# Optimization experiments

Hardware: AMD Instinct MI355X
Metric: run time of the kernel (lower is better)

The kernel has to match this reference:

```python
import jax, jax.numpy as jnp
import numpy as np

B, N, C, K = 1024, 100, 256, 3  # batch, num_proposals, hidden_dim, conv kernel size
LN_EPS = 1e-5


def setup_inputs() -> dict:
    key = jax.random.key(0)
    k1, k2, k3 = jax.random.split(key, 3)
    query = jax.random.normal(k1, (B, N, C), dtype=jnp.float32)
    value = jax.random.normal(k2, (B, N, C), dtype=jnp.float32)
    # weight_linear: Linear(hidden_dim -> kernel_size)
    W_w = jax.random.normal(k3, (K, C), dtype=jnp.float32) * (1.0 / np.sqrt(C))
    b_w = jnp.zeros((K,), dtype=jnp.float32)
    # LayerNorm(hidden_dim)
    gamma = jnp.ones((C,), dtype=jnp.float32)
    beta = jnp.zeros((C,), dtype=jnp.float32)
    return {"query": query, "value": value, "W_w": W_w, "b_w": b_w,
            "gamma": gamma, "beta": beta}


def reference(query, value, W_w, b_w, gamma, beta):
    Bq, Nq, Cq = query.shape
    Kk = W_w.shape[0]
    # dynamic depthwise kernels: [B, N, K]
    w = jnp.einsum('bnc,kc->bnk', query, W_w) + b_w
    # torch conv1d with padding='same' (cross-correlation along C, groups=N)
    pad_l = (Kk - 1) // 2
    pad_r = Kk // 2
    vpad = jnp.pad(value, ((0, 0), (0, 0), (pad_l, pad_r)))
    # sliding windows along channel axis: [B, N, C, K]
    win = jnp.stack([vpad[:, :, k:k + Cq] for k in range(Kk)], axis=-1)
    out = jnp.einsum('bnck,bnk->bnc', win, w)
    # LayerNorm over last dim
    mu = jnp.mean(out, axis=-1, keepdims=True)
    var = jnp.mean(jnp.square(out - mu), axis=-1, keepdims=True)
    out = (out - mu) * jax.lax.rsqrt(var + LN_EPS) * gamma + beta
    return out
```

## Files before the change

### kernel.cpp

```cpp
#include <hip/hip_runtime.h>

constexpr int B = 1024, N = 100, C = 256, K = 3;
constexpr int ROWS = B * N;
constexpr int THREADS = 256;
constexpr int WAVES_PER_BLOCK = THREADS / 64;
constexpr int BLOCKS = 2048;
constexpr int TOTAL_WAVES = BLOCKS * WAVES_PER_BLOCK;
constexpr float LN_EPS = 1e-5f;

typedef float f32x4 __attribute__((ext_vector_type(4)));

template <int N_>
__device__ __forceinline__ float fror(float x) {
    return __int_as_float(__builtin_amdgcn_update_dpp(
        0, __float_as_int(x), 0x120 | N_, 0xF, 0xF, false));
}

__device__ __forceinline__ float wavesum(float x) {
    x += fror<1>(x);
    x += fror<2>(x);
    x += fror<4>(x);
    x += fror<8>(x);
    x += __shfl_xor(x, 16);
    x += __shfl_xor(x, 32);
    return x;
}

__global__ __launch_bounds__(256) void dydwconv_ln_kernel(
    const float* __restrict__ query,
    const float* __restrict__ value,
    const float* __restrict__ Ww,
    const float* __restrict__ bw,
    const float* __restrict__ gamma,
    const float* __restrict__ beta,
    float* __restrict__ out)
{
    const int t    = threadIdx.x;
    const int lane = t & 63;
    const int c0   = lane * 4;
    const int row0 = blockIdx.x * WAVES_PER_BLOCK + (t >> 6);

    const int nIter = (ROWS - row0 + TOTAL_WAVES - 1) / TOTAL_WAVES;

    const float4 Wa = *(const float4*)(Ww + c0);
    const float4 Wb = *(const float4*)(Ww + C + c0);
    const float4 Wc = *(const float4*)(Ww + 2 * C + c0);
    const float4 g4 = *(const float4*)(gamma + c0);
    const float4 b4 = *(const float4*)(beta + c0);
    const float  b0 = bw[0], b1 = bw[1], b2 = bw[2];

    constexpr size_t STEP = (size_t)TOTAL_WAVES * C;
    size_t off = (size_t)row0 * C + c0;

    float4 qc = *(const float4*)(query + off);
    float4 vc = *(const float4*)(value + off);

    for (int it = 0; it < nIter; ++it) {
        const bool hn = (it + 1) < nIter;
        const size_t noff = off + STEP;
        float4 qn = qc, vn = vc;
        if (hn) {
            qn = *(const float4*)(query + noff);
            vn = *(const float4*)(value + noff);
        }

        float p0 = qc.x * Wa.x + qc.y * Wa.y + qc.z * Wa.z + qc.w * Wa.w;
        float p1 = qc.x * Wb.x + qc.y * Wb.y + qc.z * Wb.z + qc.w * Wb.w;
        float p2 = qc.x * Wc.x + qc.y * Wc.y + qc.z * Wc.z + qc.w * Wc.w;
        const float w0 = wavesum(p0) + b0;
        const float w1 = wavesum(p1) + b1;
        const float w2 = wavesum(p2) + b2;

        float vl = __shfl_up(vc.w, 1);
        float vr = __shfl_down(vc.x, 1);
        if (lane == 0)  vl = 0.0f;
        if (lane == 63) vr = 0.0f;

        const float o0 = vl   * w0 + vc.x * w1 + vc.y * w2;
        const float o1 = vc.x * w0 + vc.y * w1 + vc.z * w2;
        const float o2 = vc.y * w0 + vc.z * w1 + vc.w * w2;
        const float o3 = vc.z * w0 + vc.w * w1 + vr   * w2;

        float s  = (o0 + o1) + (o2 + o3);
        float ss = o0 * o0 + o1 * o1 + o2 * o2 + o3 * o3;
        s  = wavesum(s);
        ss = wavesum(ss);
        const float mu  = s * (1.0f / C);
        const float var = ss * (1.0f / C) - mu * mu;
        const float inv = rsqrtf(var + LN_EPS);

        f32x4 r;
        r.x = (o0 - mu) * inv * g4.x + b4.x;
        r.y = (o1 - mu) * inv * g4.y + b4.y;
        r.z = (o2 - mu) * inv * g4.z + b4.z;
        r.w = (o3 - mu) * inv * g4.w + b4.w;
        __builtin_nontemporal_store(r, (f32x4*)(out + off));

        off = noff;
        qc = qn;
        vc = vn;
    }
}

extern "C" void kernel_launch(void* const* d_in, const int* in_sizes, int n_in,
                              void* d_out, int out_size, void* d_ws, size_t ws_size,
                              hipStream_t stream) {
    const float* query = (const float*)d_in[0];
    const float* value = (const float*)d_in[1];
    const float* Ww    = (const float*)d_in[2];
    const float* bw    = (const float*)d_in[3];
    const float* gamma = (const float*)d_in[4];
    const float* beta  = (const float*)d_in[5];
    float* outp = (float*)d_out;

    dydwconv_ln_kernel<<<BLOCKS, THREADS, 0, stream>>>(
        query, value, Ww, bw, gamma, beta, outp);
}
```

Baseline: 262.6 us.

## Process four rows per wave with batched loads instead of grid-stride loop

Replaces the persistent grid-stride loop over rows with a non-persistent grid in which each wave handles four consecutive rows. All loads for those rows are issued up front, and their reductions are batched so that independent shuffles can interleave. The DPP-based wave reduction is replaced with plain shfl_xor, and nontemporal stores become regular stores. This gives more memory-level parallelism per wave, at the cost of a much larger grid, more registers, and slower shuffle-based reductions.

After: 256.5 us. 1.02x faster.

```diff
diff --git a/kernel.cpp b/kernel.cpp
--- a/kernel.cpp
+++ b/kernel.cpp
@@ -3,26 +3,15 @@
 constexpr int B = 1024, N = 100, C = 256, K = 3;
 constexpr int ROWS = B * N;
 constexpr int THREADS = 256;
-constexpr int WAVES_PER_BLOCK = THREADS / 64;
-constexpr int BLOCKS = 2048;
-constexpr int TOTAL_WAVES = BLOCKS * WAVES_PER_BLOCK;
+constexpr int WAVES_PER_BLOCK = 4;
+constexpr int RPW = 4;
+constexpr int ROWS_PER_BLOCK = WAVES_PER_BLOCK * RPW;
+constexpr int BLOCKS = ROWS / ROWS_PER_BLOCK;
 constexpr float LN_EPS = 1e-5f;
 
-typedef float f32x4 __attribute__((ext_vector_type(4)));
-
-template <int N_>
-__device__ __forceinline__ float fror(float x) {
-    return __int_as_float(__builtin_amdgcn_update_dpp(
-        0, __float_as_int(x), 0x120 | N_, 0xF, 0xF, false));
-}
-
 __device__ __forceinline__ float wavesum(float x) {
-    x += fror<1>(x);
-    x += fror<2>(x);
-    x += fror<4>(x);
-    x += fror<8>(x);
-    x += __shfl_xor(x, 16);
-    x += __shfl_xor(x, 32);
+    #pragma unroll
+    for (int off = 32; off > 0; off >>= 1) x += __shfl_xor(x, off);
     return x;
 }
 
@@ -38,9 +27,9 @@
     const int t    = threadIdx.x;
     const int lane = t & 63;
     const int c0   = lane * 4;
-    const int row0 = blockIdx.x * WAVES_PER_BLOCK + (t >> 6);
-
-    const int nIter = (ROWS - row0 + TOTAL_WAVES - 1) / TOTAL_WAVES;
+    const int wave = t >> 6;
+    const int r0   = (blockIdx.x * WAVES_PER_BLOCK + wave) * RPW;
+    const size_t base0 = (size_t)r0 * C + c0;
 
     const float4 Wa = *(const float4*)(Ww + c0);
     const float4 Wb = *(const float4*)(Ww + C + c0);
@@ -49,56 +38,63 @@
     const float4 b4 = *(const float4*)(beta + c0);
     const float  b0 = bw[0], b1 = bw[1], b2 = bw[2];
 
-    constexpr size_t STEP = (size_t)TOTAL_WAVES * C;
-    size_t off = (size_t)row0 * C + c0;
+    float4 q[RPW], v[RPW];
+    #pragma unroll
+    for (int i = 0; i < RPW; ++i) {
+        q[i] = *(const float4*)(query + base0 + (size_t)i * C);
+        v[i] = *(const float4*)(value + base0 + (size_t)i * C);
+    }
 
-    float4 qc = *(const float4*)(query + off);
-    float4 vc = *(const float4*)(value + off);
+    float p0[RPW], p1[RPW], p2[RPW];
+    #pragma unroll
+    for (int i = 0; i < RPW; ++i) {
+        p0[i] = q[i].x * Wa.x + q[i].y * Wa.y + q[i].z * Wa.z + q[i].w * Wa.w;
+        p1[i] = q[i].x * Wb.x + q[i].y * Wb.y + q[i].z * Wb.z + q[i].w * Wb.w;
+        p2[i] = q[i].x * Wc.x + q[i].y * Wc.y + q[i].z * Wc.z + q[i].w * Wc.w;
+    }
 
-    for (int it = 0; it < nIter; ++it) {
-        const bool hn = (it + 1) < nIter;
-        const size_t noff = off + STEP;
-        float4 qn = qc, vn = vc;
-        if (hn) {
-            qn = *(const float4*)(query + noff);
-            vn = *(const float4*)(value + noff);
-        }
+    float w0[RPW], w1[RPW], w2[RPW];
+    #pragma unroll
+    for (int i = 0; i < RPW; ++i) {
+        w0[i] = wavesum(p0[i]) + b0;
+        w1[i] = wavesum(p1[i]) + b1;
+        w2[i] = wavesum(p2[i]) + b2;
+    }
 
-        float p0 = qc.x * Wa.x + qc.y * Wa.y + qc.z * Wa.z + qc.w * Wa.w;
-        float p1 = qc.x * Wb.x + qc.y * Wb.y + qc.z * Wb.z + qc.w * Wb.w;
-        float p2 = qc.x * Wc.x + qc.y * Wc.y + qc.z * Wc.z + qc.w * Wc.w;
-        const float w0 = wavesum(p0) + b0;
-        const float w1 = wavesum(p1) + b1;
-        const float w2 = wavesum(p2) + b2;
-
-        float vl = __shfl_up(vc.w, 1);
-        float vr = __shfl_down(vc.x, 1);
+    float4 o[RPW];
+    float s[RPW], ss[RPW];
+    #pragma unroll
+    for (int i = 0; i < RPW; ++i) {
+        float vl = __shfl_up(v[i].w, 1);
+        float vr = __shfl_down(v[i].x, 1);
         if (lane == 0)  vl = 0.0f;
         if (lane == 63) vr = 0.0f;
+        o[i].x = vl     * w0[i] + v[i].x * w1[i] + v[i].y * w2[i];
+        o[i].y = v[i].x * w0[i] + v[i].y * w1[i] + v[i].z * w2[i];
+        o[i].z = v[i].y * w0[i] + v[i].z * w1[i] + v[i].w * w2[i];
+        o[i].w = v[i].z * w0[i] + v[i].w * w1[i] + vr     * w2[i];
+        s[i]  = (o[i].x + o[i].y) + (o[i].z + o[i].w);
+        ss[i] = o[i].x * o[i].x + o[i].y * o[i].y
+              + o[i].z * o[i].z + o[i].w * o[i].w;
+    }
 
-        const float o0 = vl   * w0 + vc.x * w1 + vc.y * w2;
-        const float o1 = vc.x * w0 + vc.y * w1 + vc.z * w2;
-        const float o2 = vc.y * w0 + vc.z * w1 + vc.w * w2;
-        const float o3 = vc.z * w0 + vc.w * w1 + vr   * w2;
+    #pragma unroll
+    for (int i = 0; i < RPW; ++i) {
+        s[i]  = wavesum(s[i]);
+        ss[i] = wavesum(ss[i]);
+    }
 
-        float s  = (o0 + o1) + (o2 + o3);
-        float ss = o0 * o0 + o1 * o1 + o2 * o2 + o3 * o3;
-        s  = wavesum(s);
-        ss = wavesum(ss);
-        const float mu  = s * (1.0f / C);
-        const float var = ss * (1.0f / C) - mu * mu;
+    #pragma unroll
+    for (int i = 0; i < RPW; ++i) {
+        const float mu  = s[i] * (1.0f / C);
+        const float var = ss[i] * (1.0f / C) - mu * mu;
         const float inv = rsqrtf(var + LN_EPS);
-
-        f32x4 r;
-        r.x = (o0 - mu) * inv * g4.x + b4.x;
-        r.y = (o1 - mu) * inv * g4.y + b4.y;
-        r.z = (o2 - mu) * inv * g4.z + b4.z;
-        r.w = (o3 - mu) * inv * g4.w + b4.w;
-        __builtin_nontemporal_store(r, (f32x4*)(out + off));
-
-        off = noff;
-        qc = qn;
-        vc = vn;
+        float4 r;
+        r.x = (o[i].x - mu) * inv * g4.x + b4.x;
+        r.y = (o[i].y - mu) * inv * g4.y + b4.y;
+        r.z = (o[i].z - mu) * inv * g4.z + b4.z;
+        r.w = (o[i].w - mu) * inv * g4.w + b4.w;
+        *(float4*)(out + base0 + (size_t)i * C) = r;
     }
 }
 
```

## Stage query/value rows into LDS with async double-buffered global_load_lds

Applied to the files above, without the earlier changes.

Each block now handles a contiguous chunk of rows rather than grid-strided ones. It copies 8 query rows and 8 value rows per step into a double-buffered shared-memory tile using the async global-to-LDS load builtin, so the next step's loads overlap the current step's compute. The DPP-based wave reduction becomes a plain shfl_xor butterfly, and output stores are no longer nontemporal. In exchange it adds block barriers and 32KB of LDS per block, and the shuffle-based reductions cost more instructions than DPP. Correctness depends on the barrier waiting for the async LDS loads to finish.

Result: slower. 276.9 us (+5.4%).

```diff
diff --git a/kernel.cpp b/kernel.cpp
--- a/kernel.cpp
+++ b/kernel.cpp
@@ -1,28 +1,18 @@
 #include <hip/hip_runtime.h>
+#include <stdint.h>
 
 constexpr int B = 1024, N = 100, C = 256, K = 3;
 constexpr int ROWS = B * N;
 constexpr int THREADS = 256;
-constexpr int WAVES_PER_BLOCK = THREADS / 64;
-constexpr int BLOCKS = 2048;
-constexpr int TOTAL_WAVES = BLOCKS * WAVES_PER_BLOCK;
+constexpr int STEP_ROWS = 8;
+constexpr int BLOCKS = 1280;
+constexpr int ROWS_PER_BLOCK = ROWS / BLOCKS;
+constexpr int NSTEPS = ROWS_PER_BLOCK / STEP_ROWS;
 constexpr float LN_EPS = 1e-5f;
 
-typedef float f32x4 __attribute__((ext_vector_type(4)));
-
-template <int N_>
-__device__ __forceinline__ float fror(float x) {
-    return __int_as_float(__builtin_amdgcn_update_dpp(
-        0, __float_as_int(x), 0x120 | N_, 0xF, 0xF, false));
-}
-
 __device__ __forceinline__ float wavesum(float x) {
-    x += fror<1>(x);
-    x += fror<2>(x);
-    x += fror<4>(x);
-    x += fror<8>(x);
-    x += __shfl_xor(x, 16);
-    x += __shfl_xor(x, 32);
+    #pragma unroll
+    for (int off = 32; off > 0; off >>= 1) x += __shfl_xor(x, off);
     return x;
 }
 
@@ -35,12 +25,13 @@
     const float* __restrict__ beta,
     float* __restrict__ out)
 {
+    __shared__ float sbuf[2][STEP_ROWS * 2 * C];
+
     const int t    = threadIdx.x;
     const int lane = t & 63;
+    const int wave = t >> 6;
     const int c0   = lane * 4;
-    const int row0 = blockIdx.x * WAVES_PER_BLOCK + (t >> 6);
-
-    const int nIter = (ROWS - row0 + TOTAL_WAVES - 1) / TOTAL_WAVES;
+    const int rowBase = blockIdx.x * ROWS_PER_BLOCK;
 
     const float4 Wa = *(const float4*)(Ww + c0);
     const float4 Wb = *(const float4*)(Ww + C + c0);
@@ -49,57 +40,73 @@
     const float4 b4 = *(const float4*)(beta + c0);
     const float  b0 = bw[0], b1 = bw[1], b2 = bw[2];
 
-    constexpr size_t STEP = (size_t)TOTAL_WAVES * C;
-    size_t off = (size_t)row0 * C + c0;
+    auto stage = [&](int buf, int step) {
+        const int r0 = rowBase + step * STEP_ROWS;
+        #pragma unroll
+        for (int k2 = 0; k2 < 4; ++k2) {
+            const int idx = wave * 4 + k2;
+            const int r   = idx & 7;
+            const float* gsrc = ((idx < 8) ? query : value)
+                              + (size_t)(r0 + r) * C + lane * 4;
+            float* ldst = &sbuf[buf][idx * C];
+            __builtin_amdgcn_global_load_lds(
+                (const __attribute__((address_space(1))) uint32_t*)gsrc,
+                (__attribute__((address_space(3))) uint32_t*)ldst,
+                16, 0, 0);
+        }
+    };
 
-    float4 qc = *(const float4*)(query + off);
-    float4 vc = *(const float4*)(value + off);
+    auto compute = [&](int buf, int step) {
+        const int r0 = rowBase + step * STEP_ROWS;
+        #pragma unroll
+        for (int rr = 0; rr < 2; ++rr) {
+            const int r = wave * 2 + rr;
+            const float4 q = *(const float4*)(&sbuf[buf][r * C] + c0);
+            const float4 v = *(const float4*)(&sbuf[buf][(STEP_ROWS + r) * C] + c0);
 
-    for (int it = 0; it < nIter; ++it) {
-        const bool hn = (it + 1) < nIter;
-        const size_t noff = off + STEP;
-        float4 qn = qc, vn = vc;
-        if (hn) {
-            qn = *(const float4*)(query + noff);
-            vn = *(const float4*)(value + noff);
+            float p0 = q.x * Wa.x + q.y * Wa.y + q.z * Wa.z + q.w * Wa.w;
+            float p1 = q.x * Wb.x + q.y * Wb.y + q.z * Wb.z + q.w * Wb.w;
+            float p2 = q.x * Wc.x + q.y * Wc.y + q.z * Wc.z + q.w * Wc.w;
+            const float w0 = wavesum(p0) + b0;
+            const float w1 = wavesum(p1) + b1;
+            const float w2 = wavesum(p2) + b2;
+
+            float vl = __shfl_up(v.w, 1);
+            float vr = __shfl_down(v.x, 1);
+            if (lane == 0)  vl = 0.0f;
+            if (lane == 63) vr = 0.0f;
+            const float o0 = vl  * w0 + v.x * w1 + v.y * w2;
+            const float o1 = v.x * w0 + v.y * w1 + v.z * w2;
+            const float o2 = v.y * w0 + v.z * w1 + v.w * w2;
+            const float o3 = v.z * w0 + v.w * w1 + vr  * w2;
+
+            float s  = (o0 + o1) + (o2 + o3);
+            float ss = o0 * o0 + o1 * o1 + o2 * o2 + o3 * o3;
+            s  = wavesum(s);
+            ss = wavesum(ss);
+            const float mu  = s * (1.0f / C);
+            const float var = ss * (1.0f / C) - mu * mu;
+            const float inv = rsqrtf(var + LN_EPS);
+
+            float4 res;
+            res.x = (o0 - mu) * inv * g4.x + b4.x;
+            res.y = (o1 - mu) * inv * g4.y + b4.y;
+            res.z = (o2 - mu) * inv * g4.z + b4.z;
+            res.w = (o3 - mu) * inv * g4.w + b4.w;
+            *(float4*)(out + (size_t)(r0 + r) * C + c0) = res;
         }
+    };
 
-        float p0 = qc.x * Wa.x + qc.y * Wa.y + qc.z * Wa.z + qc.w * Wa.w;
-        float p1 = qc.x * Wb.x + qc.y * Wb.y + qc.z * Wb.z + qc.w * Wb.w;
-        float p2 = qc.x * Wc.x + qc.y * Wc.y + qc.z * Wc.z + qc.w * Wc.w;
-        const float w0 = wavesum(p0) + b0;
-        const float w1 = wavesum(p1) + b1;
-        const float w2 = wavesum(p2) + b2;
-
-        float vl = __shfl_up(vc.w, 1);
-        float vr = __shfl_down(vc.x, 1);
-        if (lane == 0)  vl = 0.0f;
-        if (lane == 63) vr = 0.0f;
-
-        const float o0 = vl   * w0 + vc.x * w1 + vc.y * w2;
-        const float o1 = vc.x * w0 + vc.y * w1 + vc.z * w2;
-        const float o2 = vc.y * w0 + vc.z * w1 + vc.w * w2;
-        const float o3 = vc.z * w0 + vc.w * w1 + vr   * w2;
-
-        float s  = (o0 + o1) + (o2 + o3);
-        float ss = o0 * o0 + o1 * o1 + o2 * o2 + o3 * o3;
-        s  = wavesum(s);
-        ss = wavesum(ss);
-        const float mu  = s * (1.0f / C);
-        const float var = ss * (1.0f / C) - mu * mu;
-        const float inv = rsqrtf(var + LN_EPS);
-
-        f32x4 r;
-        r.x = (o0 - mu) * inv * g4.x + b4.x;
-        r.y = (o1 - mu) * inv * g4.y + b4.y;
-        r.z = (o2 - mu) * inv * g4.z + b4.z;
-        r.w = (o3 - mu) * inv * g4.w + b4.w;
-        __builtin_nontemporal_store(r, (f32x4*)(out + off));
-
-        off = noff;
-        qc = qn;
-        vc = vn;
+    stage(0, 0);
+    __syncthreads();
+    int cur = 0;
+    for (int stp = 0; stp < NSTEPS - 1; ++stp) {
+        stage(cur ^ 1, stp + 1);
+        compute(cur, stp);
+        __syncthreads();
+        cur ^= 1;
     }
+    compute(cur, NSTEPS - 1);
 }
 
 extern "C" void kernel_launch(void* const* d_in, const int* in_sizes, int n_in,
```
